# Kernel optimization log

Measured on AMD Instinct MI355X. Metric: run time of the kernel, lower is better.

## Reference

```python
import jax, jax.numpy as jnp
import numpy as np

N_NODES = 50000
N_EDGES = 800000
N_GRAPHS = 512
VOCAB = 128
HID = 64
NCLS = 5


def _seg_mean(vals, ids, num_segments):
    s = jax.ops.segment_sum(vals, ids, num_segments=num_segments)
    cnt = jax.ops.segment_sum(jnp.ones((vals.shape[0],), vals.dtype), ids, num_segments=num_segments)
    return s / jnp.maximum(cnt, 1.0)[:, None]


def sage_conv(x, src, dst, W_l, b_l, W_r):
    # PyG SAGEConv (mean aggr): out = lin_l(mean_{j in N(i)} x_j) + lin_r(x_i)
    agg = _seg_mean(x[src], dst, x.shape[0])          # [N, H] gather + scatter-mean
    return agg @ W_l.T + b_l + x @ W_r.T


def setup_inputs() -> dict:
    key = jax.random.key(0)
    ks = jax.random.split(key, 10)
    scale = 1.0 / np.sqrt(HID)
    x_tokens = jax.random.randint(ks[0], (N_NODES,), 0, VOCAB)
    edge_index = jax.random.randint(ks[1], (2, N_EDGES), 0, N_NODES)
    batch = jnp.sort(jax.random.randint(ks[2], (N_NODES,), 0, N_GRAPHS))
    return {
        "x_tokens": x_tokens,
        "edge_index": edge_index,
        "batch": batch,
        "embed": jax.random.normal(ks[3], (VOCAB, HID), jnp.float32),
        "W1l": jax.random.normal(ks[4], (HID, HID), jnp.float32) * scale,
        "b1l": jnp.zeros((HID,), jnp.float32),
        "W1r": jax.random.normal(ks[5], (HID, HID), jnp.float32) * scale,
        "W2l": jax.random.normal(ks[6], (HID, HID), jnp.float32) * scale,
        "b2l": jnp.zeros((HID,), jnp.float32),
        "W2r": jax.random.normal(ks[7], (HID, HID), jnp.float32) * scale,
        "Wlin": jax.random.normal(ks[8], (NCLS, HID), jnp.float32) * scale,
        "blin": jnp.zeros((NCLS,), jnp.float32),
    }


def reference(x_tokens, edge_index, batch, embed, W1l, b1l, W1r, W2l, b2l, W2r, Wlin, blin):
    src, dst = edge_index[0], edge_index[1]
    x = embed[x_tokens]                                  # [N, H] embedding lookup
    x = jax.nn.relu(sage_conv(x, src, dst, W1l, b1l, W1r))
    x = jax.nn.relu(sage_conv(x, src, dst, W2l, b2l, W2r))
    g = _seg_mean(x, batch, N_GRAPHS)                    # global_mean_pool -> [G, H]
    return g @ Wlin.T + blin                             # [G, num_classes]
```

## Files before the change

### kernel.cpp

```cpp
#include <hip/hip_runtime.h>

#define N_NODES  50000
#define N_EDGES  800000
#define N_GRAPHS 512
#define HID      64
#define NCLS     5
#define NB       64
#define EST      36
#define AST      68

typedef __attribute__((ext_vector_type(8))) short bf16x8;
typedef __attribute__((ext_vector_type(4))) float f32x4;

__device__ inline unsigned short f2bf(float f) {
    unsigned int u = __builtin_bit_cast(unsigned int, f);
    unsigned int r = (u + 0x7FFFu + ((u >> 16) & 1u)) >> 16;
    return (unsigned short)r;
}
__device__ inline unsigned int packbf(float a, float b) {
    return (unsigned int)f2bf(a) | ((unsigned int)f2bf(b) << 16);
}
__device__ inline float bf2f(unsigned int u16) {
    unsigned int t = u16 << 16;
    return __builtin_bit_cast(float, t);
}

#define EBUF_T (128 * 32)
#define PW_T   (64 * 64)
#define PREP_T (N_EDGES + EBUF_T + N_NODES + 2 * PW_T)
__global__ void k_prep_fill(
    const int* __restrict__ src, const int* __restrict__ dst,
    const int* __restrict__ tok,
    int* __restrict__ cnt, unsigned int* __restrict__ bucket,
    const float* __restrict__ embed, unsigned int* __restrict__ ebufg,
    const int* __restrict__ batch,
    int* __restrict__ pos_start, int* __restrict__ pos_end,
    const float* __restrict__ W1l, const float* __restrict__ W1r,
    unsigned int* __restrict__ wb1,
    const float* __restrict__ W2l, const float* __restrict__ W2r,
    unsigned int* __restrict__ wb2) {
    int gid = blockIdx.x * blockDim.x + threadIdx.x;
    if (gid < N_EDGES) {
        int s = src[gid], d = dst[gid];
        unsigned int t = (unsigned int)tok[s];
        int pos = atomicAdd(&cnt[d], 1);
        if (pos < NB) bucket[(long)d * NB + pos] = (unsigned int)s | (t << 16);
        return;
    }
    gid -= N_EDGES;
    if (gid < EBUF_T) {
        int t = gid >> 5, c = gid & 31;
        float2 v = ((const float2*)(embed + (long)t * HID))[c];
        ebufg[gid] = packbf(v.x, v.y);
        return;
    }
    gid -= EBUF_T;
    if (gid < N_NODES) {
        int n = gid;
        int b = batch[n];
        if (n == 0 || batch[n - 1] != b) pos_start[b] = n;
        if (n == N_NODES - 1 || batch[n + 1] != b) pos_end[b] = n + 1;
        return;
    }
    gid -= N_NODES;
    if (gid < 2 * PW_T) {
        const float* Wl = (gid < PW_T) ? W1l : W2l;
        const float* Wr = (gid < PW_T) ? W1r : W2r;
        unsigned int* wb = (gid < PW_T) ? wb1 : wb2;
        int i = (gid < PW_T) ? gid : gid - PW_T;
        int h = i >> 6, c = i & 63;
        float2 v = (c < 32) ? ((const float2*)(Wl + (long)h * HID))[c]
                            : ((const float2*)(Wr + (long)h * HID))[c - 32];
        wb[i] = packbf(v.x, v.y);
    }
}

template <bool L1>
__global__ __launch_bounds__(1024) void k_layer(
    const int* __restrict__ cnt, const unsigned int* __restrict__ bucket,
    const int* __restrict__ tok, const unsigned int* __restrict__ ebufg,
    const unsigned int* __restrict__ xb,
    const unsigned int* __restrict__ wb, const float* __restrict__ bl,
    unsigned short* __restrict__ xoutb)
{
    __shared__ unsigned int As[64 * AST];
    __shared__ unsigned int elds[L1 ? 128 * EST : 1];
    const int tid  = threadIdx.x;
    const int wv   = tid >> 6;
    const int lane = tid & 63;
    const int n0   = blockIdx.x * 64;

    if (L1) {
        for (int i = tid; i < EBUF_T; i += 1024) {
            int t = i >> 5, c = i & 31;
            elds[t * EST + c] = ebufg[i];
        }
        __syncthreads();
    }

    const int q  = lane & 7;
    const int e8 = lane >> 3;

#pragma unroll
    for (int i = 0; i < 4; ++i) {
        int rl = wv * 4 + i;
        int nn = n0 + rl;
        int nc = min(nn, N_NODES - 1);
        int deg = cnt[nc];
        int m   = (nn < N_NODES) ? min(deg, NB) : 0;
        unsigned int v = (lane < m) ? bucket[(long)nc * NB + lane] : 0u;
        float f0 = 0, f1 = 0, f2 = 0, f3 = 0, f4 = 0, f5 = 0, f6 = 0, f7 = 0;
#pragma unroll
        for (int g = 0; g < 8; ++g) {
            int j = g * 8 + e8;
            unsigned int vv = __shfl(v, j, 64);
            if (j < m) {
                uint4 w4;
                if (L1) w4 = *(const uint4*)(elds + (vv >> 16) * EST + q * 4);
                else    w4 = *((const uint4*)(xb + (long)(vv & 0xffffu) * 32) + q);
                f0 += bf2f(w4.x & 0xffff); f1 += bf2f(w4.x >> 16);
                f2 += bf2f(w4.y & 0xffff); f3 += bf2f(w4.y >> 16);
                f4 += bf2f(w4.z & 0xffff); f5 += bf2f(w4.z >> 16);
                f6 += bf2f(w4.w & 0xffff); f7 += bf2f(w4.w >> 16);
            }
        }
#pragma unroll
        for (int o = 8; o < 64; o <<= 1) {
            f0 += __shfl_xor(f0, o, 64); f1 += __shfl_xor(f1, o, 64);
            f2 += __shfl_xor(f2, o, 64); f3 += __shfl_xor(f3, o, 64);
            f4 += __shfl_xor(f4, o, 64); f5 += __shfl_xor(f5, o, 64);
            f6 += __shfl_xor(f6, o, 64); f7 += __shfl_xor(f7, o, 64);
        }
        if (e8 == 0) {
            float inv = 1.0f / (float)max(deg, 1);
            uint4 o;
            o.x = packbf(f0 * inv, f1 * inv);
            o.y = packbf(f2 * inv, f3 * inv);
            o.z = packbf(f4 * inv, f5 * inv);
            o.w = packbf(f6 * inv, f7 * inv);
            *(uint4*)(As + rl * AST + q * 4) = o;
        } else if (e8 == 1) {
            uint4 sv;
            if (L1) { int tk = tok[nc]; sv = *(const uint4*)(elds + tk * EST + q * 4); }
            else    { sv = *((const uint4*)(xb + (long)nc * 32) + q); }
            *(uint4*)(As + rl * AST + 32 + q * 4) = sv;
        }
    }
    __syncthreads();

    const int s    = wv & 3;
    const int t    = wv >> 2;
    const int mm   = lane & 15;
    const int quad = lane >> 4;

    bf16x8 afr[4];
#pragma unroll
    for (int kst = 0; kst < 4; ++kst)
        afr[kst] = *(const bf16x8*)(As + (s * 16 + mm) * AST + kst * 16 + quad * 4);

    f32x4 acc = (f32x4){0.f, 0.f, 0.f, 0.f};
#pragma unroll
    for (int kst = 0; kst < 4; ++kst) {
        bf16x8 bfr = *(const bf16x8*)(wb + (t * 16 + mm) * 64 + kst * 16 + quad * 4);
        acc = __builtin_amdgcn_mfma_f32_16x16x32_bf16(bfr, afr[kst], acc, 0, 0, 0);
    }

    int node = n0 + s * 16 + mm;
    if (node < N_NODES) {
        int hb = t * 16 + quad * 4;
        float4 bb = *(const float4*)(bl + hb);
        ushort4 o;
        o.x = f2bf(fmaxf(acc[0] + bb.x, 0.f));
        o.y = f2bf(fmaxf(acc[1] + bb.y, 0.f));
        o.z = f2bf(fmaxf(acc[2] + bb.z, 0.f));
        o.w = f2bf(fmaxf(acc[3] + bb.w, 0.f));
        *(ushort4*)(xoutb + (long)node * HID + hb) = o;
    }
}

__global__ __launch_bounds__(64) void k_pool(
    const unsigned int* __restrict__ x2b,
    const int* __restrict__ pos_start, const int* __restrict__ pos_end,
    const float* __restrict__ Wlin, const float* __restrict__ blin,
    float* __restrict__ out)
{
    int g    = blockIdx.x;
    int lane = threadIdx.x;
    int q    = lane & 7;
    int slot = lane >> 3;
    int s = pos_start[g], e = pos_end[g];
    float f0 = 0, f1 = 0, f2 = 0, f3 = 0, f4 = 0, f5 = 0, f6 = 0, f7 = 0;
    for (int n = s + slot; n < e; n += 8) {
        uint4 v = *((const uint4*)(x2b + (long)n * 32) + q);
        f0 += bf2f(v.x & 0xffff); f1 += bf2f(v.x >> 16);
        f2 += bf2f(v.y & 0xffff); f3 += bf2f(v.y >> 16);
        f4 += bf2f(v.z & 0xffff); f5 += bf2f(v.z >> 16);
        f6 += bf2f(v.w & 0xffff); f7 += bf2f(v.w >> 16);
    }
#pragma unroll
    for (int o = 8; o < 64; o <<= 1) {
        f0 += __shfl_xor(f0, o, 64); f1 += __shfl_xor(f1, o, 64);
        f2 += __shfl_xor(f2, o, 64); f3 += __shfl_xor(f3, o, 64);
        f4 += __shfl_xor(f4, o, 64); f5 += __shfl_xor(f5, o, 64);
        f6 += __shfl_xor(f6, o, 64); f7 += __shfl_xor(f7, o, 64);
    }
    float inv = 1.0f / (float)max(e - s, 1);
    f0 *= inv; f1 *= inv; f2 *= inv; f3 *= inv;
    f4 *= inv; f5 *= inv; f6 *= inv; f7 *= inv;
#pragma unroll
    for (int c = 0; c < NCLS; ++c) {
        const float* wr = Wlin + c * HID + q * 8;
        float p = f0 * wr[0] + f1 * wr[1] + f2 * wr[2] + f3 * wr[3] +
                  f4 * wr[4] + f5 * wr[5] + f6 * wr[6] + f7 * wr[7];
        p += __shfl_xor(p, 1, 64);
        p += __shfl_xor(p, 2, 64);
        p += __shfl_xor(p, 4, 64);
        if (lane == 0) out[g * NCLS + c] = p + blin[c];
    }
}

extern "C" void kernel_launch(void* const* d_in, const int* in_sizes, int n_in,
                              void* d_out, int out_size, void* d_ws, size_t ws_size,
                              hipStream_t stream) {
    const int*   tok   = (const int*)d_in[0];
    const int*   eidx  = (const int*)d_in[1];
    const int*   batch = (const int*)d_in[2];
    const float* embed = (const float*)d_in[3];
    const float* W1l   = (const float*)d_in[4];
    const float* b1l   = (const float*)d_in[5];
    const float* W1r   = (const float*)d_in[6];
    const float* W2l   = (const float*)d_in[7];
    const float* b2l   = (const float*)d_in[8];
    const float* W2r   = (const float*)d_in[9];
    const float* Wlin  = (const float*)d_in[10];
    const float* blin  = (const float*)d_in[11];
    float* out = (float*)d_out;

    const int* src = eidx;
    const int* dst = eidx + N_EDGES;

    char* wsp = (char*)d_ws;
    size_t off = 0;
    auto alloc = [&](size_t bytes) -> void* {
        void* p = wsp + off;
        off = (off + bytes + 255) & ~(size_t)255;
        return p;
    };
    int*   cnt     = (int*)  alloc((size_t)N_NODES * 4);
    int*   pstart  = (int*)  alloc((size_t)N_GRAPHS * 4);
    int*   pend    = (int*)  alloc((size_t)N_GRAPHS * 4);
    unsigned int* bucket = (unsigned int*)alloc((size_t)N_NODES * NB * 4);
    unsigned int* x1b    = (unsigned int*)alloc((size_t)N_NODES * 32 * 4);
    unsigned int* x2b    = (unsigned int*)alloc((size_t)N_NODES * 32 * 4);
    unsigned int* ebufg  = (unsigned int*)alloc((size_t)128 * 32 * 4);
    unsigned int* wb1    = (unsigned int*)alloc((size_t)64 * 64 * 4);
    unsigned int* wb2    = (unsigned int*)alloc((size_t)64 * 64 * 4);

    hipMemsetAsync(cnt, 0, (char*)pend - (char*)cnt + (size_t)N_GRAPHS * 4, stream);

    k_prep_fill<<<(PREP_T + 255) / 256, 256, 0, stream>>>(
        src, dst, tok, cnt, bucket,
        embed, ebufg, batch, pstart, pend, W1l, W1r, wb1, W2l, W2r, wb2);

    const int LBLK = (N_NODES + 63) / 64;
    k_layer<true><<<LBLK, 1024, 0, stream>>>(cnt, bucket, tok, ebufg, nullptr,
                                             wb1, b1l, (unsigned short*)x1b);
    k_layer<false><<<LBLK, 1024, 0, stream>>>(cnt, bucket, nullptr, nullptr, x1b,
                                              wb2, b2l, (unsigned short*)x2b);

    k_pool<<<N_GRAPHS, 64, 0, stream>>>(x2b, pstart, pend, Wlin, blin, out);
}
```

Measured before the change: 209.0 us.

## Partition edge scatter by XCD node range and widen pool to four waves

The edge bucketing pass now launches eight copies of each edge chunk, one per XCD-sized destination range, relying on round-robin block dispatch so each XCD only performs atomics and bucket writes for its own node slice. The intent is to keep the atomic counters and bucket lines local to one XCD's L2 and avoid cross-die coherence traffic. The cost is that src and dst are read eight times. The pooling kernel also uses 256 threads per graph with a shared-memory reduction, to raise memory-level parallelism per graph.

```diff
diff --git a/kernel.cpp b/kernel.cpp
--- a/kernel.cpp
+++ b/kernel.cpp
@@ -25,9 +25,13 @@
     return __builtin_bit_cast(float, t);
 }
 
+#define XCDS   8
+#define NPX    (N_NODES / XCDS)
+#define ECHUNK ((N_EDGES + 255) / 256)
+#define SEC_E  (ECHUNK * XCDS * 256)
 #define EBUF_T (128 * 32)
 #define PW_T   (64 * 64)
-#define PREP_T (N_EDGES + EBUF_T + N_NODES + 2 * PW_T)
+#define PREP_T (SEC_E + EBUF_T + N_NODES + 2 * PW_T)
 __global__ void k_prep_fill(
     const int* __restrict__ src, const int* __restrict__ dst,
     const int* __restrict__ tok,
@@ -40,14 +44,23 @@
     const float* __restrict__ W2l, const float* __restrict__ W2r,
     unsigned int* __restrict__ wb2) {
     int gid = blockIdx.x * blockDim.x + threadIdx.x;
-    if (gid < N_EDGES) {
-        int s = src[gid], d = dst[gid];
-        unsigned int t = (unsigned int)tok[s];
-        int pos = atomicAdd(&cnt[d], 1);
-        if (pos < NB) bucket[(long)d * NB + pos] = (unsigned int)s | (t << 16);
+    if (gid < SEC_E) {
+        int blk   = gid >> 8;
+        int range = blk & 7;
+        int e     = (blk >> 3) * 256 + (gid & 255);
+        if (e < N_EDGES) {
+            int d = dst[e];
+            int s = src[e];
+            int lo = range * NPX;
+            if (d >= lo && d < lo + NPX) {
+                unsigned int t = (unsigned int)tok[s];
+                int pos = atomicAdd(&cnt[d], 1);
+                if (pos < NB) bucket[(long)d * NB + pos] = (unsigned int)s | (t << 16);
+            }
+        }
         return;
     }
-    gid -= N_EDGES;
+    gid -= SEC_E;
     if (gid < EBUF_T) {
         int t = gid >> 5, c = gid & 31;
         float2 v = ((const float2*)(embed + (long)t * HID))[c];
@@ -178,19 +191,22 @@
     }
 }
 
-__global__ __launch_bounds__(64) void k_pool(
+__global__ __launch_bounds__(256) void k_pool(
     const unsigned int* __restrict__ x2b,
     const int* __restrict__ pos_start, const int* __restrict__ pos_end,
     const float* __restrict__ Wlin, const float* __restrict__ blin,
     float* __restrict__ out)
 {
+    __shared__ float part[4][8][8];
     int g    = blockIdx.x;
-    int lane = threadIdx.x;
+    int tid  = threadIdx.x;
+    int wv   = tid >> 6;
+    int lane = tid & 63;
     int q    = lane & 7;
-    int slot = lane >> 3;
+    int slot = wv * 8 + (lane >> 3);
     int s = pos_start[g], e = pos_end[g];
     float f0 = 0, f1 = 0, f2 = 0, f3 = 0, f4 = 0, f5 = 0, f6 = 0, f7 = 0;
-    for (int n = s + slot; n < e; n += 8) {
+    for (int n = s + slot; n < e; n += 32) {
         uint4 v = *((const uint4*)(x2b + (long)n * 32) + q);
         f0 += bf2f(v.x & 0xffff); f1 += bf2f(v.x >> 16);
         f2 += bf2f(v.y & 0xffff); f3 += bf2f(v.y >> 16);
@@ -204,18 +220,35 @@
         f4 += __shfl_xor(f4, o, 64); f5 += __shfl_xor(f5, o, 64);
         f6 += __shfl_xor(f6, o, 64); f7 += __shfl_xor(f7, o, 64);
     }
-    float inv = 1.0f / (float)max(e - s, 1);
-    f0 *= inv; f1 *= inv; f2 *= inv; f3 *= inv;
-    f4 *= inv; f5 *= inv; f6 *= inv; f7 *= inv;
-#pragma unroll
-    for (int c = 0; c < NCLS; ++c) {
-        const float* wr = Wlin + c * HID + q * 8;
-        float p = f0 * wr[0] + f1 * wr[1] + f2 * wr[2] + f3 * wr[3] +
-                  f4 * wr[4] + f5 * wr[5] + f6 * wr[6] + f7 * wr[7];
-        p += __shfl_xor(p, 1, 64);
-        p += __shfl_xor(p, 2, 64);
-        p += __shfl_xor(p, 4, 64);
-        if (lane == 0) out[g * NCLS + c] = p + blin[c];
+    if (lane < 8) {
+        part[wv][lane][0] = f0; part[wv][lane][1] = f1;
+        part[wv][lane][2] = f2; part[wv][lane][3] = f3;
+        part[wv][lane][4] = f4; part[wv][lane][5] = f5;
+        part[wv][lane][6] = f6; part[wv][lane][7] = f7;
+    }
+    __syncthreads();
+    if (wv == 0) {
+        f0 = part[0][q][0] + part[1][q][0] + part[2][q][0] + part[3][q][0];
+        f1 = part[0][q][1] + part[1][q][1] + part[2][q][1] + part[3][q][1];
+        f2 = part[0][q][2] + part[1][q][2] + part[2][q][2] + part[3][q][2];
+        f3 = part[0][q][3] + part[1][q][3] + part[2][q][3] + part[3][q][3];
+        f4 = part[0][q][4] + part[1][q][4] + part[2][q][4] + part[3][q][4];
+        f5 = part[0][q][5] + part[1][q][5] + part[2][q][5] + part[3][q][5];
+        f6 = part[0][q][6] + part[1][q][6] + part[2][q][6] + part[3][q][6];
+        f7 = part[0][q][7] + part[1][q][7] + part[2][q][7] + part[3][q][7];
+        float inv = 1.0f / (float)max(e - s, 1);
+        f0 *= inv; f1 *= inv; f2 *= inv; f3 *= inv;
+        f4 *= inv; f5 *= inv; f6 *= inv; f7 *= inv;
+#pragma unroll
+        for (int c = 0; c < NCLS; ++c) {
+            const float* wr = Wlin + c * HID + q * 8;
+            float p = f0 * wr[0] + f1 * wr[1] + f2 * wr[2] + f3 * wr[3] +
+                      f4 * wr[4] + f5 * wr[5] + f6 * wr[6] + f7 * wr[7];
+            p += __shfl_xor(p, 1, 64);
+            p += __shfl_xor(p, 2, 64);
+            p += __shfl_xor(p, 4, 64);
+            if (lane == 0) out[g * NCLS + c] = p + blin[c];
+        }
     }
 }
 
@@ -268,5 +301,5 @@
     k_layer<false><<<LBLK, 1024, 0, stream>>>(cnt, bucket, nullptr, nullptr, x1b,
                                               wb2, b2l, (unsigned short*)x2b);
 
-    k_pool<<<N_GRAPHS, 64, 0, stream>>>(x2b, pstart, pend, Wlin, blin, out);
-}
+    k_pool<<<N_GRAPHS, 256, 0, stream>>>(x2b, pstart, pend, Wlin, blin, out);
+}
```

Measured after the change: 203.5 us. -2.6%, faster.
